# Kernel optimization log

Measured on AMD Instinct MI355X. Metric: run time of the kernel, lower is better.

Reference implementation:

```python
import jax, jax.numpy as jnp
import numpy as np

NEG_INF = -jnp.inf


def setup_inputs() -> dict:
    key = jax.random.key(0)
    ks = jax.random.split(key, 6)
    B, S, D, DK = 8, 2048, 1024, 128
    x = jax.random.normal(ks[0], (B, S, D), dtype=jnp.float32)
    context = jax.random.normal(ks[1], (B, S, D), dtype=jnp.float32)
    # torch nn.Linear weights: [out_features, in_features]
    Wq = jax.random.normal(ks[2], (DK, D), dtype=jnp.float32) * 0.02
    Wk = jax.random.normal(ks[3], (DK, D), dtype=jnp.float32) * 0.02
    Wv = jax.random.normal(ks[4], (DK, D), dtype=jnp.float32) * 0.02
    # valid lengths in [S//2, S] so every row has at least one valid key
    batch_lengths = jax.random.randint(ks[5], (B,), S // 2, S + 1, dtype=jnp.int32)
    return {
        "x": x,
        "context": context,
        "Wq": Wq,
        "Wk": Wk,
        "Wv": Wv,
        "batch_lengths": batch_lengths,
        "max_len": S,
        "decoding": 1,
    }


def reference(x, context, Wq, Wk, Wv, batch_lengths, max_len, decoding):
    B, S, D = x.shape
    dk = Wq.shape[0]
    pos = jnp.arange(S)
    # outputMask: 1.0 for t < length, else 0.0; broadcast over feature dim dk
    valid = pos[None, :] < batch_lengths[:, None]            # [B, S]
    mask = valid[:, :, None].astype(x.dtype)                 # [B, S, 1] (broadcast to dk)
    Q = jnp.einsum('bsd,kd->bsk', context, Wq) * mask        # [B, S, dk]
    K = jnp.einsum('bsd,kd->bsk', context, Wk) * mask
    V = jnp.einsum('bsd,kd->bsk', x, Wv) * mask
    energy = jnp.einsum('bqk,bjk->bqj', Q, K)                # [B, S, S]
    # attnMask: -inf at padded key positions (j >= length)
    key_pad = ~valid                                         # [B, S]
    energy = jnp.where(key_pad[:, None, :], NEG_INF, energy)
    if decoding:
        # causal: energy[:, i, j] = -inf for j > i (the python double loop)
        causal = pos[:, None] < pos[None, :]                 # [S, S], True above diag
        energy = jnp.where(causal[None, :, :], NEG_INF, energy)
    score = jax.nn.softmax(energy / jnp.sqrt(jnp.asarray(dk, x.dtype)), axis=-1)
    return jnp.einsum('bqj,bjk->bqk', score, V)              # [B, S, dk]
```

## Files before the change

### kernel.cpp

```cpp
#include <hip/hip_runtime.h>
#include <hip/hip_bf16.h>

#define BB 8
#define SS 2048
#define DD 1024
#define DKK 128

using bf16x8  = __attribute__((ext_vector_type(8))) __bf16;
using floatx4 = __attribute__((ext_vector_type(4))) float;
using intx4   = __attribute__((ext_vector_type(4))) int;

__device__ __forceinline__ void lds16(const void* g, void* l) {
    __builtin_amdgcn_global_load_lds((const __attribute__((address_space(1))) void*)g,
                                     (__attribute__((address_space(3))) void*)l, 16, 0, 0);
}

__device__ __forceinline__ int pack2(float a, float b) {
    union { __bf16 h; unsigned short u; } ua, ub;
    ua.h = (__bf16)a; ub.h = (__bf16)b;
    return (int)(ua.u | ((unsigned)ub.u << 16));
}

__global__ __launch_bounds__(256) void convw_kernel(
    const float* __restrict__ Wq, const float* __restrict__ Wk,
    const float* __restrict__ Wv, __bf16* __restrict__ Wt)
{
    const int z = blockIdx.y;
    const float* W = (z == 0) ? Wq : (z == 1) ? Wk : Wv;
    const int t  = blockIdx.x * 256 + threadIdx.x;
    const int n  = t >> 7;
    const int k0 = (t & 127) * 8;
    float4 f0 = *(const float4*)(W + n * DD + k0);
    float4 f1 = *(const float4*)(W + n * DD + k0 + 4);
    bf16x8 v;
    v[0]=(__bf16)f0.x; v[1]=(__bf16)f0.y; v[2]=(__bf16)f0.z; v[3]=(__bf16)f0.w;
    v[4]=(__bf16)f1.x; v[5]=(__bf16)f1.y; v[6]=(__bf16)f1.z; v[7]=(__bf16)f1.w;
    const int kb  = (k0 >> 3) & 7;
    const int kbs = kb ^ (n & 7);
    *(bf16x8*)(Wt + (size_t)z * 131072 + ((k0 >> 6) * 128 + n) * 64 + kbs * 8) = v;
}

__global__ __launch_bounds__(256, 2) void proj_kernel(
    const float* __restrict__ x, const float* __restrict__ ctx,
    const __bf16* __restrict__ Wt, const int* __restrict__ lengths,
    __bf16* __restrict__ Qb, __bf16* __restrict__ Kb, __bf16* __restrict__ Vt)
{
    __shared__ __align__(16) __bf16 SH[20992];
    __bf16* Abuf = SH;
    __bf16* Wl0  = SH + 4608;
    __bf16* Wl1  = SH + 12800;
    __bf16* T    = SH + 4608;

    const int isV = blockIdx.x >= 256;
    const int m0  = (isV ? blockIdx.x - 256 : blockIdx.x) * 64;
    const int b   = m0 >> 11;
    const int s0  = m0 & (SS - 1);
    const int len = lengths[b];
    if (s0 >= len) return;

    const int tid  = threadIdx.x;
    const int wave = tid >> 6;
    const int lane = tid & 63;
    const int quad = lane >> 4;
    const int l16  = lane & 15;
    const int wm   = wave >> 1;
    const int wn   = wave & 1;

    const float*  A  = isV ? x : ctx;
    const __bf16* W0 = isV ? (Wt + 262144) : Wt;
    const __bf16* W1 = Wt + 131072;

    const int r    = tid >> 2;
    const int kseg = (tid & 3) * 16;
    const float* Ab = A + (size_t)(m0 + r) * DD + kseg;

    floatx4 acc[2][2][4];
#pragma unroll
    for (int m_ = 0; m_ < 2; ++m_)
#pragma unroll
        for (int i = 0; i < 2; ++i)
#pragma unroll
            for (int j = 0; j < 4; ++j) acc[m_][i][j] = (floatx4){0.f,0.f,0.f,0.f};

    float4 pf[4];
#pragma unroll
    for (int i = 0; i < 4; ++i) pf[i] = *(const float4*)(Ab + i * 4);

    for (int t = 0; t < 16; ++t) {
        __syncthreads();
        {
            bf16x8 c0, c1;
            c0[0]=(__bf16)pf[0].x; c0[1]=(__bf16)pf[0].y; c0[2]=(__bf16)pf[0].z; c0[3]=(__bf16)pf[0].w;
            c0[4]=(__bf16)pf[1].x; c0[5]=(__bf16)pf[1].y; c0[6]=(__bf16)pf[1].z; c0[7]=(__bf16)pf[1].w;
            c1[0]=(__bf16)pf[2].x; c1[1]=(__bf16)pf[2].y; c1[2]=(__bf16)pf[2].z; c1[3]=(__bf16)pf[2].w;
            c1[4]=(__bf16)pf[3].x; c1[5]=(__bf16)pf[3].y; c1[6]=(__bf16)pf[3].z; c1[7]=(__bf16)pf[3].w;
            *(bf16x8*)&Abuf[r * 72 + kseg]     = c0;
            *(bf16x8*)&Abuf[r * 72 + kseg + 8] = c1;
        }
#pragma unroll
        for (int i = 0; i < 4; ++i) {
            const int c = wave * 4 + i;
            lds16(W0 + (size_t)t * 8192 + c * 512 + lane * 8, Wl0 + c * 512);
            if (!isV)
                lds16(W1 + (size_t)t * 8192 + c * 512 + lane * 8, Wl1 + c * 512);
        }
        if (t < 15) {
            const float* ap = Ab + (t + 1) * 64;
#pragma unroll
            for (int i = 0; i < 4; ++i) pf[i] = *(const float4*)(ap + i * 4);
        }
        __syncthreads();

#pragma unroll
        for (int kh = 0; kh < 2; ++kh) {
            bf16x8 af[2];
#pragma unroll
            for (int mt = 0; mt < 2; ++mt)
                af[mt] = *(const bf16x8*)&Abuf[(wm*32 + mt*16 + l16) * 72 + kh*32 + quad*8];
            const int kb = kh * 4 + quad;
#pragma unroll
            for (int nt = 0; nt < 4; ++nt) {
                const int n = wn * 64 + nt * 16 + l16;
                const int off = n * 64 + ((kb ^ (n & 7)) << 3);
                bf16x8 w0 = *(const bf16x8*)&Wl0[off];
#pragma unroll
                for (int mt = 0; mt < 2; ++mt)
                    acc[0][mt][nt] = __builtin_amdgcn_mfma_f32_16x16x32_bf16(af[mt], w0, acc[0][mt][nt], 0, 0, 0);
                if (!isV) {
                    bf16x8 w1 = *(const bf16x8*)&Wl1[off];
#pragma unroll
                    for (int mt = 0; mt < 2; ++mt)
                        acc[1][mt][nt] = __builtin_amdgcn_mfma_f32_16x16x32_bf16(af[mt], w1, acc[1][mt][nt], 0, 0, 0);
                }
            }
        }
    }

    if (!isV) {
#pragma unroll
        for (int mt = 0; mt < 2; ++mt)
#pragma unroll
            for (int rr = 0; rr < 4; ++rr) {
                const int row = m0 + wm*32 + mt*16 + quad*4 + rr;
                const float mk = ((row & (SS - 1)) < len) ? 1.f : 0.f;
#pragma unroll
                for (int nt = 0; nt < 4; ++nt) {
                    const int col = wn*64 + nt*16 + l16;
                    Qb[(size_t)row * DKK + col] = (__bf16)(acc[0][mt][nt][rr] * mk);
                    Kb[(size_t)row * DKK + col] = (__bf16)(acc[1][mt][nt][rr] * mk);
                }
            }
    } else {
        __syncthreads();
#pragma unroll
        for (int mt = 0; mt < 2; ++mt)
#pragma unroll
            for (int nt = 0; nt < 4; ++nt)
#pragma unroll
                for (int rr = 0; rr < 4; ++rr) {
                    const int s = wm*32 + mt*16 + quad*4 + rr;
                    const int n = wn*64 + nt*16 + l16;
                    const float mk = (s0 + s < len) ? 1.f : 0.f;
                    T[n * 72 + s] = (__bf16)(acc[0][mt][nt][rr] * mk);
                }
        __syncthreads();
        const int n = tid >> 1, h = tid & 1;
        __bf16* dst = Vt + (size_t)b * DKK * SS + (size_t)n * SS + s0 + h * 32;
#pragma unroll
        for (int i = 0; i < 4; ++i)
            *(bf16x8*)(dst + i * 8) = *(const bf16x8*)&T[n * 72 + h * 32 + i * 8];
    }
}

__global__ __launch_bounds__(256) void vmean_kernel(
    const __bf16* __restrict__ Vt, const int* __restrict__ lengths,
    float* __restrict__ Vmean)
{
    const int b   = blockIdx.x >> 3;
    const int g3  = blockIdx.x & 7;
    const int len = lengths[b];
    const int tid = threadIdx.x;
    const int n   = g3 * 16 + (tid >> 4);
    const int sl  = (tid & 15) * 128;
    const __bf16* src = Vt + (size_t)b * DKK * SS + (size_t)n * SS + sl;
    float s = 0.f;
#pragma unroll
    for (int i = 0; i < 16; ++i) {
        bf16x8 v = *(const bf16x8*)(src + i * 8);
#pragma unroll
        for (int j = 0; j < 8; ++j)
            s += (sl + i * 8 + j < len) ? (float)v[j] : 0.f;
    }
#pragma unroll
    for (int off = 1; off < 16; off <<= 1)
        s += __shfl_xor(s, off, 64);
    if ((tid & 15) == 0) Vmean[b * DKK + n] = s / (float)len;
}

__global__ __launch_bounds__(256) void attn_kernel(
    const __bf16* __restrict__ Qb, const __bf16* __restrict__ Kb,
    const __bf16* __restrict__ Vt, const int* __restrict__ lengths,
    const float* __restrict__ Vmean, float* __restrict__ out)
{
    __shared__ __align__(16) __bf16 KB[2 * 8192];
    __shared__ __align__(16) __bf16 VB[2 * 8192];

    const int b    = blockIdx.x & 7;
    const int qt   = 31 - (blockIdx.x >> 3);
    const int qw   = qt * 64;
    const int len  = lengths[b];
    const int tid  = threadIdx.x;
    const int wave = tid >> 6;
    const int lane = tid & 63;
    const int quad = lane >> 4;
    const int l16  = lane & 15;

    if (qw >= len) {
        const int c8 = (tid & 15) * 8;
        const float4 v0 = *(const float4*)(Vmean + b * DKK + c8);
        const float4 v1 = *(const float4*)(Vmean + b * DKK + c8 + 4);
#pragma unroll
        for (int pass = 0; pass < 4; ++pass) {
            const int row = pass * 16 + (tid >> 4);
            float* op = out + (size_t)(b * SS + qw + row) * DKK + c8;
            *(float4*)op = v0; *(float4*)(op + 4) = v1;
        }
        return;
    }

    const int jmax = min(qw + 64, len);
    const int nc   = (jmax + 63) >> 6;
    const __bf16* Kbase = Kb + (size_t)b * SS * DKK;
    const __bf16* Vbase = Vt + (size_t)b * DKK * SS;

    bf16x8 qfrag[4];
    {
        const __bf16* Qbase = Qb + (size_t)(b * SS + qw + wave * 16) * DKK;
#pragma unroll
        for (int cc = 0; cc < 4; ++cc)
            qfrag[cc] = *(const bf16x8*)(Qbase + (size_t)l16 * DKK + cc * 32 + quad * 8);
    }

    floatx4 oacc[8];
#pragma unroll
    for (int nt = 0; nt < 8; ++nt) oacc[nt] = (floatx4){0.f,0.f,0.f,0.f};
    float lsum = 0.f;
    const float scale = 0.08838834764831845f;
    const int   iq    = qw + wave * 16 + l16;
    const int   sw7   = l16 & 7;

    auto stageK = [&](int buf, int j0) {
#pragma unroll
        for (int i = 0; i < 4; ++i) {
            const int c   = wave * 4 + i;
            const int row = c * 4 + quad;
            const int sb  = l16 ^ (row & 7);
            lds16(Kbase + (size_t)(j0 + row) * DKK + sb * 8,
                  KB + buf * 8192 + c * 512);
        }
    };
    auto stageV = [&](int buf, int j0) {
#pragma unroll
        for (int i = 0; i < 4; ++i) {
            const int c   = wave * 4 + i;
            const int row = c * 8 + (lane >> 3);
            const int sb  = (lane & 7) ^ (row & 7);
            lds16(Vbase + (size_t)row * SS + j0 + sb * 8,
                  VB + buf * 8192 + c * 512);
        }
    };

    auto process = [&](int buf, int j0) {
        const int kbas = buf * 8192;
        floatx4 st[4];
#pragma unroll
        for (int jt = 0; jt < 4; ++jt) {
            st[jt] = (floatx4){0.f,0.f,0.f,0.f};
#pragma unroll
            for (int cc = 0; cc < 4; ++cc) {
                bf16x8 kf = *(const bf16x8*)(
                    KB + kbas + (jt*16 + l16) * 128 + (((cc*4 + quad) ^ sw7) * 8));
                st[jt] = __builtin_amdgcn_mfma_f32_16x16x32_bf16(
                    kf, qfrag[cc], st[jt], 0, 0, 0);
            }
        }
        int pk[4][2];
#pragma unroll
        for (int jt = 0; jt < 4; ++jt) {
            float p[4];
#pragma unroll
            for (int rr = 0; rr < 4; ++rr) {
                const int j = j0 + jt*16 + quad*4 + rr;
                p[rr] = (j > iq || j >= len) ? 0.f : __expf(st[jt][rr] * scale - 8.f);
                lsum += p[rr];
            }
            pk[jt][0] = pack2(p[0], p[1]);
            pk[jt][1] = pack2(p[2], p[3]);
        }
        const int a0 = (((quad & 1) << 5) + l16) << 2;
        const int a1 = a0 + 64;
#pragma unroll
        for (int f = 0; f < 2; ++f) {
            const int r00 = __builtin_amdgcn_ds_bpermute(a0, pk[2*f  ][0]);
            const int r01 = __builtin_amdgcn_ds_bpermute(a0, pk[2*f  ][1]);
            const int r02 = __builtin_amdgcn_ds_bpermute(a0, pk[2*f+1][0]);
            const int r03 = __builtin_amdgcn_ds_bpermute(a0, pk[2*f+1][1]);
            const int r10 = __builtin_amdgcn_ds_bpermute(a1, pk[2*f  ][0]);
            const int r11 = __builtin_amdgcn_ds_bpermute(a1, pk[2*f  ][1]);
            const int r12 = __builtin_amdgcn_ds_bpermute(a1, pk[2*f+1][0]);
            const int r13 = __builtin_amdgcn_ds_bpermute(a1, pk[2*f+1][1]);
            const bool hi = quad >= 2;
            union { intx4 i; bf16x8 h; } u;
            u.i = (intx4){ hi ? r02 : r00, hi ? r03 : r01,
                           hi ? r12 : r10, hi ? r13 : r11 };
#pragma unroll
            for (int nt = 0; nt < 8; ++nt) {
                bf16x8 vf = *(const bf16x8*)(
                    VB + kbas + (nt*16 + l16) * 64 + (((f*4 + quad) ^ sw7) * 8));
                oacc[nt] = __builtin_amdgcn_mfma_f32_16x16x32_bf16(
                    u.h, vf, oacc[nt], 0, 0, 0);
            }
        }
    };

    stageK(0, 0); stageV(0, 0);
    __syncthreads();
    for (int c = 0; c < nc; ++c) {
        const int cur = c & 1;
        if (c + 1 < nc) { stageK(cur ^ 1, (c + 1) * 64); stageV(cur ^ 1, (c + 1) * 64); }
        process(cur, c * 64);
        __syncthreads();
    }

    lsum += __shfl_xor(lsum, 16, 64);
    lsum += __shfl_xor(lsum, 32, 64);
    float inv[4];
#pragma unroll
    for (int rr = 0; rr < 4; ++rr)
        inv[rr] = 1.f / __shfl(lsum, quad * 4 + rr, 64);
#pragma unroll
    for (int nt = 0; nt < 8; ++nt)
#pragma unroll
        for (int rr = 0; rr < 4; ++rr)
            out[(size_t)(b * SS + qw + wave*16 + quad*4 + rr) * DKK + nt*16 + l16] =
                oacc[nt][rr] * inv[rr];
}

extern "C" void kernel_launch(void* const* d_in, const int* in_sizes, int n_in,
                              void* d_out, int out_size, void* d_ws, size_t ws_size,
                              hipStream_t stream) {
    const float* x   = (const float*)d_in[0];
    const float* ctx = (const float*)d_in[1];
    const float* Wq  = (const float*)d_in[2];
    const float* Wk  = (const float*)d_in[3];
    const float* Wv  = (const float*)d_in[4];
    const int* lengths = (const int*)d_in[5];
    float* out = (float*)d_out;

    char* ws = (char*)d_ws;
    __bf16* Wt = (__bf16*)ws;
    __bf16* Qb = (__bf16*)(ws + 786432);
    __bf16* Kb = (__bf16*)(ws + 786432 + 4194304);
    __bf16* Vt = (__bf16*)(ws + 786432 + 8388608);
    float*  Vm = (float*) (ws + 786432 + 12582912);

    convw_kernel<<<dim3(64, 3), 256, 0, stream>>>(Wq, Wk, Wv, Wt);
    proj_kernel<<<512, 256, 0, stream>>>(x, ctx, Wt, lengths, Qb, Kb, Vt);
    vmean_kernel<<<64, 256, 0, stream>>>(Vt, lengths, Vm);
    attn_kernel<<<256, 256, 0, stream>>>(Qb, Kb, Vt, lengths, Vm, out);
}
```

Baseline: 227.3 us.

## Halve query tile and split key chunk across wave pairs with LDS reduction

The attention kernel now handles 32 query rows per block instead of 64 and launches 512 blocks. Each pair of waves shares a 16-row query slice, and each wave of the pair covers half of every 64-key chunk. The partial outputs and row sums are combined through LDS at the end. The aim is more blocks and finer load balance across CUs for the causal workload. The cost is K/V being staged twice as often per query row, plus an extra LDS reduction and barrier.

```diff
diff --git a/kernel.cpp b/kernel.cpp
--- a/kernel.cpp
+++ b/kernel.cpp
@@ -206,21 +206,23 @@
     __shared__ __align__(16) __bf16 VB[2 * 8192];
 
     const int b    = blockIdx.x & 7;
-    const int qt   = 31 - (blockIdx.x >> 3);
-    const int qw   = qt * 64;
+    const int qt   = 63 - (blockIdx.x >> 3);
+    const int qw   = qt * 32;
     const int len  = lengths[b];
     const int tid  = threadIdx.x;
     const int wave = tid >> 6;
     const int lane = tid & 63;
     const int quad = lane >> 4;
     const int l16  = lane & 15;
+    const int sub  = wave >> 1;
+    const int half = wave & 1;
 
     if (qw >= len) {
         const int c8 = (tid & 15) * 8;
         const float4 v0 = *(const float4*)(Vmean + b * DKK + c8);
         const float4 v1 = *(const float4*)(Vmean + b * DKK + c8 + 4);
 #pragma unroll
-        for (int pass = 0; pass < 4; ++pass) {
+        for (int pass = 0; pass < 2; ++pass) {
             const int row = pass * 16 + (tid >> 4);
             float* op = out + (size_t)(b * SS + qw + row) * DKK + c8;
             *(float4*)op = v0; *(float4*)(op + 4) = v1;
@@ -228,14 +230,14 @@
         return;
     }
 
-    const int jmax = min(qw + 64, len);
+    const int jmax = min(qw + 32, len);
     const int nc   = (jmax + 63) >> 6;
     const __bf16* Kbase = Kb + (size_t)b * SS * DKK;
     const __bf16* Vbase = Vt + (size_t)b * DKK * SS;
 
     bf16x8 qfrag[4];
     {
-        const __bf16* Qbase = Qb + (size_t)(b * SS + qw + wave * 16) * DKK;
+        const __bf16* Qbase = Qb + (size_t)(b * SS + qw + sub * 16) * DKK;
 #pragma unroll
         for (int cc = 0; cc < 4; ++cc)
             qfrag[cc] = *(const bf16x8*)(Qbase + (size_t)l16 * DKK + cc * 32 + quad * 8);
@@ -246,7 +248,7 @@
     for (int nt = 0; nt < 8; ++nt) oacc[nt] = (floatx4){0.f,0.f,0.f,0.f};
     float lsum = 0.f;
     const float scale = 0.08838834764831845f;
-    const int   iq    = qw + wave * 16 + l16;
+    const int   iq    = qw + sub * 16 + l16;
     const int   sw7   = l16 & 7;
 
     auto stageK = [&](int buf, int j0) {
@@ -272,25 +274,25 @@
 
     auto process = [&](int buf, int j0) {
         const int kbas = buf * 8192;
-        floatx4 st[4];
-#pragma unroll
-        for (int jt = 0; jt < 4; ++jt) {
+        floatx4 st[2];
+#pragma unroll
+        for (int jt = 0; jt < 2; ++jt) {
             st[jt] = (floatx4){0.f,0.f,0.f,0.f};
 #pragma unroll
             for (int cc = 0; cc < 4; ++cc) {
                 bf16x8 kf = *(const bf16x8*)(
-                    KB + kbas + (jt*16 + l16) * 128 + (((cc*4 + quad) ^ sw7) * 8));
+                    KB + kbas + ((half*2 + jt)*16 + l16) * 128 + (((cc*4 + quad) ^ sw7) * 8));
                 st[jt] = __builtin_amdgcn_mfma_f32_16x16x32_bf16(
                     kf, qfrag[cc], st[jt], 0, 0, 0);
             }
         }
-        int pk[4][2];
-#pragma unroll
-        for (int jt = 0; jt < 4; ++jt) {
+        int pk[2][2];
+#pragma unroll
+        for (int jt = 0; jt < 2; ++jt) {
             float p[4];
 #pragma unroll
             for (int rr = 0; rr < 4; ++rr) {
-                const int j = j0 + jt*16 + quad*4 + rr;
+                const int j = j0 + half*32 + jt*16 + quad*4 + rr;
                 p[rr] = (j > iq || j >= len) ? 0.f : __expf(st[jt][rr] * scale - 8.f);
                 lsum += p[rr];
             }
@@ -299,27 +301,24 @@
         }
         const int a0 = (((quad & 1) << 5) + l16) << 2;
         const int a1 = a0 + 64;
-#pragma unroll
-        for (int f = 0; f < 2; ++f) {
-            const int r00 = __builtin_amdgcn_ds_bpermute(a0, pk[2*f  ][0]);
-            const int r01 = __builtin_amdgcn_ds_bpermute(a0, pk[2*f  ][1]);
-            const int r02 = __builtin_amdgcn_ds_bpermute(a0, pk[2*f+1][0]);
-            const int r03 = __builtin_amdgcn_ds_bpermute(a0, pk[2*f+1][1]);
-            const int r10 = __builtin_amdgcn_ds_bpermute(a1, pk[2*f  ][0]);
-            const int r11 = __builtin_amdgcn_ds_bpermute(a1, pk[2*f  ][1]);
-            const int r12 = __builtin_amdgcn_ds_bpermute(a1, pk[2*f+1][0]);
-            const int r13 = __builtin_amdgcn_ds_bpermute(a1, pk[2*f+1][1]);
-            const bool hi = quad >= 2;
-            union { intx4 i; bf16x8 h; } u;
-            u.i = (intx4){ hi ? r02 : r00, hi ? r03 : r01,
-                           hi ? r12 : r10, hi ? r13 : r11 };
-#pragma unroll
-            for (int nt = 0; nt < 8; ++nt) {
-                bf16x8 vf = *(const bf16x8*)(
-                    VB + kbas + (nt*16 + l16) * 64 + (((f*4 + quad) ^ sw7) * 8));
-                oacc[nt] = __builtin_amdgcn_mfma_f32_16x16x32_bf16(
-                    u.h, vf, oacc[nt], 0, 0, 0);
-            }
+        const int r00 = __builtin_amdgcn_ds_bpermute(a0, pk[0][0]);
+        const int r01 = __builtin_amdgcn_ds_bpermute(a0, pk[0][1]);
+        const int r02 = __builtin_amdgcn_ds_bpermute(a0, pk[1][0]);
+        const int r03 = __builtin_amdgcn_ds_bpermute(a0, pk[1][1]);
+        const int r10 = __builtin_amdgcn_ds_bpermute(a1, pk[0][0]);
+        const int r11 = __builtin_amdgcn_ds_bpermute(a1, pk[0][1]);
+        const int r12 = __builtin_amdgcn_ds_bpermute(a1, pk[1][0]);
+        const int r13 = __builtin_amdgcn_ds_bpermute(a1, pk[1][1]);
+        const bool hi = quad >= 2;
+        union { intx4 i; bf16x8 h; } u;
+        u.i = (intx4){ hi ? r02 : r00, hi ? r03 : r01,
+                       hi ? r12 : r10, hi ? r13 : r11 };
+#pragma unroll
+        for (int nt = 0; nt < 8; ++nt) {
+            bf16x8 vf = *(const bf16x8*)(
+                VB + kbas + (nt*16 + l16) * 64 + (((half*4 + quad) ^ sw7) * 8));
+            oacc[nt] = __builtin_amdgcn_mfma_f32_16x16x32_bf16(
+                u.h, vf, oacc[nt], 0, 0, 0);
         }
     };
 
@@ -334,16 +333,31 @@
 
     lsum += __shfl_xor(lsum, 16, 64);
     lsum += __shfl_xor(lsum, 32, 64);
-    float inv[4];
-#pragma unroll
-    for (int rr = 0; rr < 4; ++rr)
-        inv[rr] = 1.f / __shfl(lsum, quad * 4 + rr, 64);
-#pragma unroll
-    for (int nt = 0; nt < 8; ++nt)
+
+    float* Ored = (float*)KB;
+    float* Lred = (float*)VB;
+    if (half) {
+#pragma unroll
+        for (int nt = 0; nt < 8; ++nt)
+#pragma unroll
+            for (int rr = 0; rr < 4; ++rr)
+                Ored[sub*2048 + (quad*4 + rr)*128 + nt*16 + l16] = oacc[nt][rr];
+        if (lane < 16) Lred[sub*16 + l16] = lsum;
+    }
+    __syncthreads();
+    if (!half) {
+        const float lt = lsum + Lred[sub*16 + l16];
+        float inv[4];
 #pragma unroll
         for (int rr = 0; rr < 4; ++rr)
-            out[(size_t)(b * SS + qw + wave*16 + quad*4 + rr) * DKK + nt*16 + l16] =
-                oacc[nt][rr] * inv[rr];
+            inv[rr] = 1.f / __shfl(lt, quad * 4 + rr, 64);
+#pragma unroll
+        for (int nt = 0; nt < 8; ++nt)
+#pragma unroll
+            for (int rr = 0; rr < 4; ++rr)
+                out[(size_t)(b * SS + qw + sub*16 + quad*4 + rr) * DKK + nt*16 + l16] =
+                    (oacc[nt][rr] + Ored[sub*2048 + (quad*4 + rr)*128 + nt*16 + l16]) * inv[rr];
+    }
 }
 
 extern "C" void kernel_launch(void* const* d_in, const int* in_sizes, int n_in,
@@ -367,5 +381,5 @@
     convw_kernel<<<dim3(64, 3), 256, 0, stream>>>(Wq, Wk, Wv, Wt);
     proj_kernel<<<512, 256, 0, stream>>>(x, ctx, Wt, lengths, Qb, Kb, Vt);
     vmean_kernel<<<64, 256, 0, stream>>>(Vt, lengths, Vm);
-    attn_kernel<<<256, 256, 0, stream>>>(Qb, Kb, Vt, lengths, Vm, out);
-}
+    attn_kernel<<<512, 256, 0, stream>>>(Qb, Kb, Vt, lengths, Vm, out);
+}
```

Result: faster. 215.5 us (-5.2%).
